# Kernel optimization log

Hardware: AMD Instinct MI355X
Metric: run time of the kernel (lower is better)

The kernel has to match this reference:

```python
import jax, jax.numpy as jnp
import numpy as np

B, IMG, TXT = 1, 2048, 256
D_MODEL = 2048
HEADS, HEAD_DIM = 16, 128
INNER = HEADS * HEAD_DIM
EPS = 1e-5
SCALE = HEAD_DIM ** -0.5


def _rmsnorm(x, w):
    # normalize over last dim (head_dim)
    return (x * jax.lax.rsqrt(jnp.mean(x * x, axis=-1, keepdims=True) + EPS)) * w


def _rope(x, cos, sin):
    # x: (B, S, H, D); cos/sin: (S, D) with pairwise-repeated freqs (interleaved convention)
    c = cos[None, :, None, :]
    s = sin[None, :, None, :]
    x1 = x[..., 0::2]
    x2 = x[..., 1::2]
    rot = jnp.stack([-x2, x1], axis=-1).reshape(x.shape)
    return x * c + rot * s


def setup_inputs() -> dict:
    key = jax.random.key(0)
    ks = jax.random.split(key, 12)
    sc_in = D_MODEL ** -0.5
    sc_inner = INNER ** -0.5
    inp = {
        'hidden_states': jax.random.normal(ks[0], (B, IMG, D_MODEL), jnp.float32),
        'encoder_hidden_states': jax.random.normal(ks[1], (B, TXT, D_MODEL), jnp.float32),
    }
    # RoPE tables over the joint (text + image) sequence, interleaved pair layout
    pos = jnp.arange(TXT + IMG, dtype=jnp.float32)
    inv = 1.0 / (10000.0 ** (jnp.arange(0, HEAD_DIM, 2, dtype=jnp.float32) / HEAD_DIM))
    freqs = pos[:, None] * inv[None, :]
    freqs = jnp.repeat(freqs, 2, axis=-1)  # (S, HEAD_DIM)
    inp['freqs_cos'] = jnp.cos(freqs)
    inp['freqs_sin'] = jnp.sin(freqs)
    # parameters (stored (in, out))
    inp['Wqkv'] = jax.random.normal(ks[2], (D_MODEL, 3 * INNER), jnp.float32) * sc_in
    inp['Wqkv_add'] = jax.random.normal(ks[3], (D_MODEL, 3 * INNER), jnp.float32) * sc_in
    inp['b_qkv_add'] = jax.random.normal(ks[4], (3 * INNER,), jnp.float32) * 0.01
    inp['norm_q_w'] = jnp.ones((HEAD_DIM,), jnp.float32)
    inp['norm_k_w'] = jnp.ones((HEAD_DIM,), jnp.float32)
    inp['norm_aq_w'] = jnp.ones((HEAD_DIM,), jnp.float32)
    inp['norm_ak_w'] = jnp.ones((HEAD_DIM,), jnp.float32)
    inp['Wout'] = jax.random.normal(ks[5], (INNER, D_MODEL), jnp.float32) * sc_inner
    inp['b_out'] = jax.random.normal(ks[6], (D_MODEL,), jnp.float32) * 0.01
    inp['Wadd_out'] = jax.random.normal(ks[7], (INNER, D_MODEL), jnp.float32) * sc_inner
    inp['b_add_out'] = jax.random.normal(ks[8], (D_MODEL,), jnp.float32) * 0.01
    return inp


def reference(hidden_states, encoder_hidden_states, freqs_cos, freqs_sin,
              Wqkv, Wqkv_add, b_qkv_add, norm_q_w, norm_k_w, norm_aq_w, norm_ak_w,
              Wout, b_out, Wadd_out, b_add_out):
    b, s_img, _ = hidden_states.shape
    s_txt = encoder_hidden_states.shape[1]

    # fused QKV projection (image stream), chunk q/k/v, unflatten heads
    qkv = hidden_states @ Wqkv  # (B, IMG, 3*INNER)
    q, k, v = jnp.split(qkv, 3, axis=-1)
    q = _rmsnorm(q.reshape(b, s_img, HEADS, HEAD_DIM), norm_q_w)
    k = _rmsnorm(k.reshape(b, s_img, HEADS, HEAD_DIM), norm_k_w)
    v = v.reshape(b, s_img, HEADS, HEAD_DIM)

    # fused QKV projection (text stream, with bias)
    eqkv = encoder_hidden_states @ Wqkv_add + b_qkv_add
    eq, ek, ev = jnp.split(eqkv, 3, axis=-1)
    eq = _rmsnorm(eq.reshape(b, s_txt, HEADS, HEAD_DIM), norm_aq_w)
    ek = _rmsnorm(ek.reshape(b, s_txt, HEADS, HEAD_DIM), norm_ak_w)
    ev = ev.reshape(b, s_txt, HEADS, HEAD_DIM)

    # joint [text; image] concatenation, then RoPE on joint Q/K
    jq = jnp.concatenate([eq, q], axis=1)
    jk = jnp.concatenate([ek, k], axis=1)
    jv = jnp.concatenate([ev, v], axis=1)
    jq = _rope(jq, freqs_cos, freqs_sin)
    jk = _rope(jk, freqs_cos, freqs_sin)

    # non-causal scaled dot-product attention, layout (B, S, H, D)
    scores = jnp.einsum('bqhd,bkhd->bhqk', jq, jk) * SCALE
    probs = jax.nn.softmax(scores, axis=-1)
    out = jnp.einsum('bhqk,bkhd->bqhd', probs, jv)  # (B, S_joint, H, D)
    out = out.reshape(b, s_txt + s_img, INNER)

    enc_out = out[:, :s_txt]
    img_out = out[:, s_txt:]
    img_out = img_out @ Wout + b_out
    enc_out = enc_out @ Wadd_out + b_add_out
    return (img_out, enc_out)
```

## Files before the change

kernel.cpp:

```cpp
#include <hip/hip_runtime.h>
#include <stdint.h>

#define HEADS 16
#define HD 128
#define S_TXT 256
#define S_IMG 2048
#define S_ALL 2304
#define DMODEL 2048
#define N_QKV 6144
#define INNER 2048
#define ATT_EPS 1e-5f
#define ATT_SCALE 0.08838834764831845f
#define LOG2E 1.4426950408889634f
#define MBOUND 16.5f
#define QT_N 18
#define TPS 36

typedef __attribute__((ext_vector_type(8))) __bf16 bf16x8;
typedef __attribute__((ext_vector_type(4))) float f32x4;
typedef __attribute__((ext_vector_type(4))) uint32_t u32x4;

__device__ __forceinline__ uint16_t f2bf(float f) {
  union { float f; uint32_t u; } v; v.f = f;
  uint32_t r = (v.u + 0x7FFF + ((v.u >> 16) & 1)) >> 16;
  return (uint16_t)r;
}
__device__ __forceinline__ float bf2f(uint16_t h) {
  union { float f; uint32_t u; } v; v.u = ((uint32_t)h) << 16;
  return v.f;
}
__device__ __forceinline__ float fexp2(float x) {
#if __has_builtin(__builtin_amdgcn_exp2f)
  return __builtin_amdgcn_exp2f(x);
#else
  return __expf(x * 0.69314718055994531f);
#endif
}

__device__ __forceinline__ void async_cp16(const void* g, void* l) {
  __builtin_amdgcn_global_load_lds(
      (const __attribute__((address_space(1))) void*)g,
      (__attribute__((address_space(3))) void*)l, 16, 0, 0);
}

__global__ __launch_bounds__(256) void k_cvt2(
    const float* __restrict__ s0, uint16_t* __restrict__ d0, int n40,
    const float* __restrict__ s1, uint16_t* __restrict__ d1, int n41) {
  const float* src; uint16_t* dst; int n4, bid, nb;
  if (blockIdx.x < 1024) { src = s0; dst = d0; n4 = n40; bid = blockIdx.x; nb = 1024; }
  else { src = s1; dst = d1; n4 = n41; bid = blockIdx.x - 1024; nb = 128; }
  int i = bid * 256 + threadIdx.x;
  int stride = nb * 256;
  for (; i < n4; i += stride) {
    float4 v = ((const float4*)src)[i];
    uint16_t o[4];
    o[0] = f2bf(v.x); o[1] = f2bf(v.y); o[2] = f2bf(v.z); o[3] = f2bf(v.w);
    ((uint2*)dst)[i] = *(const uint2*)o;
  }
}

__global__ __launch_bounds__(256) void k_cvt_t4(
    const float* __restrict__ s0, uint16_t* __restrict__ d0,
    const float* __restrict__ s1, uint16_t* __restrict__ d1,
    const float* __restrict__ s2, uint16_t* __restrict__ d2,
    const float* __restrict__ s3, uint16_t* __restrict__ d3) {
  __shared__ float t[64][65];
  int b = blockIdx.x;
  const float* src; uint16_t* dst; int R, C, tb;
  if (b < 3072)      { src = s0; dst = d0; R = DMODEL; C = N_QKV;  tb = b; }
  else if (b < 6144) { src = s1; dst = d1; R = DMODEL; C = N_QKV;  tb = b - 3072; }
  else if (b < 7168) { src = s2; dst = d2; R = INNER;  C = DMODEL; tb = b - 6144; }
  else               { src = s3; dst = d3; R = INNER;  C = DMODEL; tb = b - 7168; }
  int ntr = R >> 6;
  int tr = tb % ntr, tc = tb / ntr;
  int tid = threadIdx.x;
  int rr = tid >> 4, c4 = (tid & 15) * 4;
#pragma unroll
  for (int j = 0; j < 4; ++j) {
    int r = rr + j * 16;
    float4 v = *(const float4*)&src[(size_t)(tr * 64 + r) * C + tc * 64 + c4];
    *(float4*)&t[r][c4] = v;
  }
  __syncthreads();
  int cc = tid >> 4, r4 = (tid & 15) * 4;
#pragma unroll
  for (int j = 0; j < 4; ++j) {
    int c = cc + j * 16;
    uint16_t ov[4];
    ov[0] = f2bf(t[r4 + 0][c]); ov[1] = f2bf(t[r4 + 1][c]);
    ov[2] = f2bf(t[r4 + 2][c]); ov[3] = f2bf(t[r4 + 3][c]);
    *(uint2*)&dst[(size_t)(tc * 64 + c) * R + tr * 64 + r4] = *(const uint2*)ov;
  }
}

__global__ __launch_bounds__(512, 1) void k_gemm2(
    const uint16_t* __restrict__ A0, const uint16_t* __restrict__ B0,
    const float* __restrict__ bias0, uint16_t* __restrict__ C0,
    const uint16_t* __restrict__ A1, const uint16_t* __restrict__ B1,
    const float* __restrict__ bias1, uint16_t* __restrict__ C1,
    int seg0_tiles, int N, int K) {
  __shared__ __align__(16) char lds[2 * 65536];
  int bn = blockIdx.x, bm = blockIdx.y;
  const uint16_t* A; const uint16_t* B; const float* bias; uint16_t* C; int mrow;
  if (bm < seg0_tiles) { A = A0; B = B0; bias = bias0; C = C0; mrow = bm * 256; }
  else { A = A1; B = B1; bias = bias1; C = C1; mrow = (bm - seg0_tiles) * 256; }
  int tid = threadIdx.x, lane = tid & 63, w = tid >> 6;
  int g = lane >> 4, li = lane & 15;
  int wm = w >> 2, wn = w & 3;
  const int NKI = K / 64;

  int rowin = lane >> 3;
  int csrc = (lane & 7) ^ rowin;

  auto stage = [&](int t, char* buf) {
    int kt = t * 64;
#pragma unroll
    for (int j = 0; j < 4; ++j) {
      int r = w * 4 + j;
      int tr = r * 8 + rowin;
      async_cp16(A + (size_t)(mrow + tr) * K + kt + 8 * csrc, buf + r * 1024);
    }
#pragma unroll
    for (int j = 0; j < 4; ++j) {
      int r = w * 4 + j;
      int tr = r * 8 + rowin;
      async_cp16(B + (size_t)(bn * 256 + tr) * K + kt + 8 * csrc, buf + 32768 + r * 1024);
    }
  };

  f32x4 acc[8][4] = {};

  stage(0, lds);
  asm volatile("s_waitcnt vmcnt(0)" ::: "memory");
  __builtin_amdgcn_s_barrier();
  asm volatile("" ::: "memory");

  for (int t = 0; t < NKI; ++t) {
    const char* cur = lds + (t & 1) * 65536;
    if (t + 1 < NKI) stage(t + 1, lds + ((t + 1) & 1) * 65536);

#pragma unroll
    for (int kk = 0; kk < 2; ++kk) {
      bf16x8 af[8], bfv[4];
#pragma unroll
      for (int mi = 0; mi < 8; ++mi) {
        int row = wm * 128 + mi * 16 + li;
        int ch = (kk * 4 + g) ^ (row & 7);
        af[mi] = __builtin_bit_cast(bf16x8, *(const u32x4*)(cur + row * 128 + ch * 16));
      }
#pragma unroll
      for (int ni = 0; ni < 4; ++ni) {
        int row = wn * 64 + ni * 16 + li;
        int ch = (kk * 4 + g) ^ (row & 7);
        bfv[ni] = __builtin_bit_cast(bf16x8, *(const u32x4*)(cur + 32768 + row * 128 + ch * 16));
      }
      __builtin_amdgcn_s_setprio(1);
#pragma unroll
      for (int mi = 0; mi < 8; ++mi)
#pragma unroll
        for (int ni = 0; ni < 4; ++ni)
          acc[mi][ni] = __builtin_amdgcn_mfma_f32_16x16x32_bf16(af[mi], bfv[ni], acc[mi][ni], 0, 0, 0);
      __builtin_amdgcn_s_setprio(0);
    }

    if (t + 1 < NKI) {
      asm volatile("s_waitcnt vmcnt(0)" ::: "memory");
      __builtin_amdgcn_s_barrier();
      asm volatile("" ::: "memory");
    }
  }

#pragma unroll
  for (int mi = 0; mi < 8; ++mi) {
#pragma unroll
    for (int ni = 0; ni < 4; ++ni) {
      int col = bn * 256 + wn * 64 + ni * 16 + li;
      float bv = bias ? bias[col] : 0.0f;
#pragma unroll
      for (int i = 0; i < 4; ++i) {
        int r = mrow + wm * 128 + mi * 16 + 4 * g + i;
        C[(size_t)r * N + col] = f2bf(acc[mi][ni][i] + bv);
      }
    }
  }
}

__global__ __launch_bounds__(256, 4) void k_gemmO(
    const uint16_t* __restrict__ A0, const uint16_t* __restrict__ B0,
    const float* __restrict__ bias0, float* __restrict__ C0,
    const uint16_t* __restrict__ A1, const uint16_t* __restrict__ B1,
    const float* __restrict__ bias1, float* __restrict__ C1,
    int seg0_tiles, int N, int K) {
  __shared__ __align__(16) char lds[4 * 8192];
  int bn = blockIdx.x, bm = blockIdx.y;
  const uint16_t* A; const uint16_t* B; const float* bias; float* C; int mrow;
  if (bm < seg0_tiles) { A = A0; B = B0; bias = bias0; C = C0; mrow = bm * 128; }
  else { A = A1; B = B1; bias = bias1; C = C1; mrow = (bm - seg0_tiles) * 128; }
  int tid = threadIdx.x, lane = tid & 63, w = tid >> 6;
  int g = lane >> 4, li = lane & 15;
  int wm = w >> 1, wn = w & 1;
  const int NKT = K / 32;

  int rowin = lane >> 2;
  int csrc = (lane & 3) ^ (rowin & 3);

  auto stage = [&](int t, int buf) {
    int kt = t * 32;
#pragma unroll
    for (int j = 0; j < 2; ++j) {
      int r = w * 2 + j;
      int tr = r * 16 + rowin;
      async_cp16(A + (size_t)(mrow + tr) * K + kt + 8 * csrc, lds + buf * 8192 + r * 1024);
    }
#pragma unroll
    for (int j = 0; j < 2; ++j) {
      int r = w * 2 + j;
      int tr = r * 16 + rowin;
      async_cp16(B + (size_t)(bn * 128 + tr) * K + kt + 8 * csrc, lds + 16384 + buf * 8192 + r * 1024);
    }
  };

  f32x4 acc[4][4] = {};
  stage(0, 0);
  asm volatile("s_waitcnt vmcnt(0)" ::: "memory");
  __builtin_amdgcn_s_barrier();
  asm volatile("" ::: "memory");

  for (int t = 0; t < NKT; ++t) {
    int cur = t & 1;
    bool pre = (t + 1 < NKT);
    if (pre) stage(t + 1, cur ^ 1);
    const char* Ac = lds + cur * 8192;
    const char* Bc = lds + 16384 + cur * 8192;

    bf16x8 af[4], bfv[4];
#pragma unroll
    for (int mi = 0; mi < 4; ++mi) {
      int row = wm * 64 + mi * 16 + li;
      af[mi] = __builtin_bit_cast(bf16x8, *(const u32x4*)(Ac + row * 64 + (g ^ (row & 3)) * 16));
    }
#pragma unroll
    for (int ni = 0; ni < 4; ++ni) {
      int row = wn * 64 + ni * 16 + li;
      bfv[ni] = __builtin_bit_cast(bf16x8, *(const u32x4*)(Bc + row * 64 + (g ^ (row & 3)) * 16));
    }
    __builtin_amdgcn_s_setprio(1);
#pragma unroll
    for (int mi = 0; mi < 4; ++mi)
#pragma unroll
      for (int ni = 0; ni < 4; ++ni)
        acc[mi][ni] = __builtin_amdgcn_mfma_f32_16x16x32_bf16(af[mi], bfv[ni], acc[mi][ni], 0, 0, 0);
    __builtin_amdgcn_s_setprio(0);

    if (pre) asm volatile("s_waitcnt vmcnt(0)" ::: "memory");
    __builtin_amdgcn_s_barrier();
    asm volatile("" ::: "memory");
  }

#pragma unroll
  for (int mi = 0; mi < 4; ++mi) {
#pragma unroll
    for (int ni = 0; ni < 4; ++ni) {
      int col = bn * 128 + wn * 64 + ni * 16 + li;
      float bv = bias[col];
#pragma unroll
      for (int i = 0; i < 4; ++i) {
        int r = mrow + wm * 64 + mi * 16 + 4 * g + i;
        C[(size_t)r * N + col] = acc[mi][ni][i] + bv;
      }
    }
  }
}

__global__ __launch_bounds__(256) void k_postvt(
    const uint16_t* __restrict__ qkv_img, const uint16_t* __restrict__ qkv_txt,
    const float* __restrict__ fcos, const float* __restrict__ fsin,
    const float* __restrict__ wq, const float* __restrict__ wk,
    const float* __restrict__ waq, const float* __restrict__ wak,
    uint16_t* __restrict__ Qo, uint16_t* __restrict__ Ko, uint16_t* __restrict__ VTo) {
  __shared__ uint16_t Vl[64][136];
  if (blockIdx.x < S_ALL) {
    int s = blockIdx.x;
    const uint16_t* row = (s < S_TXT) ? qkv_txt + (size_t)s * N_QKV
                                      : qkv_img + (size_t)(s - S_TXT) * N_QKV;
    const float* wqp = (s < S_TXT) ? waq : wq;
    const float* wkp = (s < S_TXT) ? wak : wk;
    int lane = threadIdx.x & 63, w = threadIdx.x >> 6;
    int h = w * 4 + (lane >> 4);
    int d0 = (lane & 15) * 8;
    float cs[8], sn[8];
#pragma unroll
    for (int j = 0; j < 8; ++j) {
      cs[j] = fcos[s * HD + d0 + j];
      sn[j] = fsin[s * HD + d0 + j];
    }
#pragma unroll
    for (int part = 0; part < 2; ++part) {
      const uint16_t* src = row + part * INNER + h * HD + d0;
      u32x4 raw = *(const u32x4*)src;
      const uint16_t* rp = (const uint16_t*)&raw;
      float x[8], ss = 0.f;
#pragma unroll
      for (int j = 0; j < 8; ++j) { x[j] = bf2f(rp[j]); ss += x[j] * x[j]; }
      ss += __shfl_xor(ss, 1); ss += __shfl_xor(ss, 2);
      ss += __shfl_xor(ss, 4); ss += __shfl_xor(ss, 8);
      float rn = rsqrtf(ss * (1.0f / HD) + ATT_EPS);
      const float* wp = part ? wkp : wqp;
#pragma unroll
      for (int j = 0; j < 8; ++j) x[j] = x[j] * rn * wp[d0 + j];
      float y[8];
#pragma unroll
      for (int j = 0; j < 8; j += 2) {
        y[j]     = x[j] * cs[j] - x[j + 1] * sn[j];
        y[j + 1] = x[j + 1] * cs[j + 1] + x[j] * sn[j + 1];
      }
      float sc = part ? 1.0f : (ATT_SCALE * LOG2E);
      uint16_t ov[8];
#pragma unroll
      for (int j = 0; j < 8; ++j) ov[j] = f2bf(y[j] * sc);
      uint16_t* dst = (part ? Ko : Qo) + ((size_t)h * S_ALL + s) * HD + d0;
      *(u32x4*)dst = *(const u32x4*)ov;
    }
  } else {
    int b = blockIdx.x - S_ALL;
    int st = b % 36, h = b / 36;
    int s0 = st * 64;
    const uint16_t* base = (s0 < S_TXT) ? qkv_txt + (size_t)s0 * N_QKV
                                        : qkv_img + (size_t)(s0 - S_TXT) * N_QKV;
    base += 2 * INNER + h * HD;
    int tid = threadIdx.x;
#pragma unroll
    for (int it = 0; it < 4; ++it) {
      int idx = it * 256 + tid;
      int r = idx >> 4, c = idx & 15;
      *(u32x4*)&Vl[r][c * 8] = *(const u32x4*)(base + (size_t)r * N_QKV + c * 8);
    }
    __syncthreads();
#pragma unroll
    for (int it = 0; it < 4; ++it) {
      int idx = it * 256 + tid;
      int d = idx >> 3, sc = (idx & 7) * 8;
      uint16_t tmp[8];
#pragma unroll
      for (int j = 0; j < 8; ++j) tmp[j] = Vl[sc + j][d];
      *(u32x4*)&VTo[((size_t)h * HD + d) * S_ALL + s0 + sc] = *(const u32x4*)tmp;
    }
  }
}

__global__ __launch_bounds__(256, 3) void k_attn(
    const uint16_t* __restrict__ Qg, const uint16_t* __restrict__ Kg,
    const uint16_t* __restrict__ VTg,
    uint16_t* __restrict__ part0, uint16_t* __restrict__ part1,
    float* __restrict__ lsumP) {
  __shared__ __align__(16) char Kt[2][8192];
  __shared__ __align__(16) char Vt[2][8192];
  __shared__ __align__(16) uint16_t Pl[4][32 * 40];

  int b0 = blockIdx.x;
  int bid = (b0 & 7) * 72 + (b0 >> 3);
  int h = bid / 36, r6 = bid % 36, sp = r6 / 18, qt = r6 % 18;
  int tid = threadIdx.x, lane = tid & 63, w = tid >> 6;
  int g = lane >> 4, li = lane & 15;

  const uint16_t* Kh = Kg + (size_t)h * S_ALL * HD;
  const uint16_t* Vh = VTg + (size_t)h * HD * S_ALL;
  uint16_t* po = (sp ? part1 : part0) + ((size_t)(h * QT_N + qt) * 128 + w * 32) * 128;

  int qbase = qt * 128 + w * 32;
  bf16x8 qf[2][4];
#pragma unroll
  for (int q2 = 0; q2 < 2; ++q2) {
    const uint16_t* qp = Qg + ((size_t)h * S_ALL + qbase + q2 * 16 + li) * HD;
#pragma unroll
    for (int kc = 0; kc < 4; ++kc)
      qf[q2][kc] = __builtin_bit_cast(bf16x8, *(const u32x4*)(qp + kc * 32 + g * 8));
  }
  f32x4 o[2][8] = {};
  float lsum[2] = {0.f, 0.f};

  auto stage = [&](int tk, int buf) {
#pragma unroll
    for (int j = 0; j < 2; ++j) {
      int cj = w * 128 + j * 64 + lane;
      int row = cj >> 4, c = (cj & 15) ^ (row & 15);
      async_cp16(Kh + (size_t)(tk * 32 + row) * HD + 8 * c, Kt[buf] + (w * 128 + j * 64) * 16);
    }
#pragma unroll
    for (int j = 0; j < 2; ++j) {
      int cj = w * 128 + j * 64 + lane;
      int row = cj >> 2, c = (cj & 3) ^ ((row >> 1) & 3);
      async_cp16(Vh + (size_t)row * S_ALL + tk * 32 + 8 * c, Vt[buf] + (w * 128 + j * 64) * 16);
    }
  };

  int t0 = sp * TPS;
  stage(t0, 0);
  asm volatile("s_waitcnt vmcnt(0)" ::: "memory");
  __builtin_amdgcn_s_barrier();
  asm volatile("" ::: "memory");

  for (int t = 0; t < TPS; ++t) {
    int cur = t & 1;
    if (t + 1 < TPS) stage(t0 + t + 1, cur ^ 1);
    const char* KtC = Kt[cur];
    const char* VtC = Vt[cur];

    f32x4 sc[2][2];
#pragma unroll
    for (int q2 = 0; q2 < 2; ++q2)
#pragma unroll
      for (int kb = 0; kb < 2; ++kb)
        sc[q2][kb] = (f32x4){-MBOUND, -MBOUND, -MBOUND, -MBOUND};
    __builtin_amdgcn_s_setprio(1);
#pragma unroll
    for (int kb = 0; kb < 2; ++kb)
#pragma unroll
      for (int kc = 0; kc < 4; ++kc) {
        int ch = (kc * 4 + g) ^ li;
        bf16x8 kf = __builtin_bit_cast(bf16x8,
            *(const u32x4*)(KtC + (kb * 16 + li) * 256 + ch * 16));
        sc[0][kb] = __builtin_amdgcn_mfma_f32_16x16x32_bf16(kf, qf[0][kc], sc[0][kb], 0, 0, 0);
        sc[1][kb] = __builtin_amdgcn_mfma_f32_16x16x32_bf16(kf, qf[1][kc], sc[1][kb], 0, 0, 0);
      }
    __builtin_amdgcn_s_setprio(0);

    uint16_t* Pw = &Pl[w][0];
#pragma unroll
    for (int q2 = 0; q2 < 2; ++q2)
#pragma unroll
      for (int kb = 0; kb < 2; ++kb) {
        float p0 = fexp2(sc[q2][kb][0]);
        float p1 = fexp2(sc[q2][kb][1]);
        float p2 = fexp2(sc[q2][kb][2]);
        float p3 = fexp2(sc[q2][kb][3]);
        lsum[q2] += (p0 + p1) + (p2 + p3);
        uint2 pk;
        pk.x = (uint32_t)f2bf(p0) | ((uint32_t)f2bf(p1) << 16);
        pk.y = (uint32_t)f2bf(p2) | ((uint32_t)f2bf(p3) << 16);
        *(uint2*)((char*)Pw + (q2 * 16 + li) * 80 + kb * 32 + g * 8) = pk;
      }

    bf16x8 pf[2];
#pragma unroll
    for (int q2 = 0; q2 < 2; ++q2)
      pf[q2] = __builtin_bit_cast(bf16x8,
          *(const u32x4*)((const char*)Pw + (q2 * 16 + li) * 80 + g * 16));
    __builtin_amdgcn_s_setprio(1);
#pragma unroll
    for (int db = 0; db < 8; ++db) {
      int vrow = db * 16 + li;
      int ch = g ^ ((vrow >> 1) & 3);
      bf16x8 vf = __builtin_bit_cast(bf16x8, *(const u32x4*)(VtC + vrow * 64 + ch * 16));
      o[0][db] = __builtin_amdgcn_mfma_f32_16x16x32_bf16(pf[0], vf, o[0][db], 0, 0, 0);
      o[1][db] = __builtin_amdgcn_mfma_f32_16x16x32_bf16(pf[1], vf, o[1][db], 0, 0, 0);
    }
    __builtin_amdgcn_s_setprio(0);

    asm volatile("s_waitcnt vmcnt(0)" ::: "memory");
    __builtin_amdgcn_s_barrier();
    asm volatile("" ::: "memory");
  }

#pragma unroll
  for (int q2 = 0; q2 < 2; ++q2) {
    float v = lsum[q2];
    v += __shfl_xor(v, 16);
    v += __shfl_xor(v, 32);
    lsum[q2] = v;
  }
  if (lane < 16) {
#pragma unroll
    for (int q2 = 0; q2 < 2; ++q2)
      lsumP[((size_t)sp * HEADS + h) * S_ALL + qbase + q2 * 16 + lane] = lsum[q2];
  }
#pragma unroll
  for (int q2 = 0; q2 < 2; ++q2)
#pragma unroll
    for (int db = 0; db < 8; ++db)
#pragma unroll
      for (int i = 0; i < 4; ++i)
        po[(q2 * 16 + 4 * g + i) * 128 + db * 16 + li] = f2bf(o[q2][db][i]);
}

__global__ __launch_bounds__(256) void k_comb(
    const uint16_t* __restrict__ p0, const uint16_t* __restrict__ p1,
    const float* __restrict__ lsumP, uint16_t* __restrict__ attn) {
  int q = blockIdx.x, qt = q >> 7, ql = q & 127;
#pragma unroll
  for (int rep = 0; rep < 2; ++rep) {
    int d4 = threadIdx.x + rep * 256;
    int d = d4 * 4, h = d >> 7, dl = d & 127;
    size_t off = (((size_t)h * QT_N + qt) * 128 + ql) * 128 + dl;
    uint2 a = *(const uint2*)&p0[off];
    uint2 b = *(const uint2*)&p1[off];
    const uint16_t* ap = (const uint16_t*)&a;
    const uint16_t* bp = (const uint16_t*)&b;
    float l0 = lsumP[(size_t)h * S_ALL + q];
    float l1 = lsumP[((size_t)HEADS + h) * S_ALL + q];
    float inv = 1.0f / (l0 + l1);
    uint16_t ov[4];
#pragma unroll
    for (int j = 0; j < 4; ++j)
      ov[j] = f2bf((bf2f(ap[j]) + bf2f(bp[j])) * inv);
    *(uint2*)&attn[(size_t)q * INNER + d] = *(const uint2*)ov;
  }
}

extern "C" void kernel_launch(void* const* d_in, const int* in_sizes, int n_in,
                              void* d_out, int out_size, void* d_ws, size_t ws_size,
                              hipStream_t stream) {
  const float* hidden = (const float*)d_in[0];
  const float* enc    = (const float*)d_in[1];
  const float* fcos   = (const float*)d_in[2];
  const float* fsin   = (const float*)d_in[3];
  const float* Wqkv   = (const float*)d_in[4];
  const float* Wqkva  = (const float*)d_in[5];
  const float* bqkva  = (const float*)d_in[6];
  const float* nqw    = (const float*)d_in[7];
  const float* nkw    = (const float*)d_in[8];
  const float* naqw   = (const float*)d_in[9];
  const float* nakw   = (const float*)d_in[10];
  const float* Wout   = (const float*)d_in[11];
  const float* bout   = (const float*)d_in[12];
  const float* Wadd   = (const float*)d_in[13];
  const float* badd   = (const float*)d_in[14];
  float* out_img = (float*)d_out;
  float* out_enc = (float*)d_out + (size_t)S_IMG * DMODEL;

  char* ws = (char*)d_ws;
  size_t off = 0;
  auto alloc = [&](size_t bytes) {
    char* p = ws + off;
    off += (bytes + 255) & ~(size_t)255;
    return p;
  };
  uint16_t* hs_bf   = (uint16_t*)alloc((size_t)S_IMG * DMODEL * 2);
  uint16_t* enc_bf  = (uint16_t*)alloc((size_t)S_TXT * DMODEL * 2);
  char*     wqkv_base = alloc((size_t)N_QKV * DMODEL * 2 * 2);
  uint16_t* WqkvT   = (uint16_t*)wqkv_base;
  uint16_t* WqkvaT  = (uint16_t*)(wqkv_base + (size_t)N_QKV * DMODEL * 2);
  uint16_t* WoutT   = (uint16_t*)alloc((size_t)DMODEL * INNER * 2);
  uint16_t* WaddT   = (uint16_t*)alloc((size_t)DMODEL * INNER * 2);
  uint16_t* qkv_img = (uint16_t*)alloc((size_t)S_IMG * N_QKV * 2);
  uint16_t* qkv_txt = (uint16_t*)alloc((size_t)S_TXT * N_QKV * 2);
  uint16_t* Qb   = (uint16_t*)wqkv_base;
  uint16_t* Kb   = Qb + (size_t)HEADS * S_ALL * HD;
  uint16_t* VTb  = Kb + (size_t)HEADS * S_ALL * HD;
  uint16_t* attn = VTb + (size_t)HEADS * S_ALL * HD;
  uint16_t* part0 = (uint16_t*)d_out;
  uint16_t* part1 = (uint16_t*)qkv_img;
  float* lsumP = (float*)enc_bf;

  k_cvt2<<<1152, 256, 0, stream>>>(hidden, hs_bf, S_IMG * DMODEL / 4,
                                   enc, enc_bf, S_TXT * DMODEL / 4);
  k_cvt_t4<<<8192, 256, 0, stream>>>(Wqkv, WqkvT, Wqkva, WqkvaT, Wout, WoutT, Wadd, WaddT);

  dim3 gq(N_QKV / 256, (S_TXT + S_IMG) / 256);
  k_gemm2<<<gq, 512, 0, stream>>>(enc_bf, WqkvaT, bqkva, qkv_txt,
                                  hs_bf, WqkvT, nullptr, qkv_img,
                                  1, N_QKV, DMODEL);

  k_postvt<<<S_ALL + 36 * HEADS, 256, 0, stream>>>(qkv_img, qkv_txt, fcos, fsin,
                                                   nqw, nkw, naqw, nakw, Qb, Kb, VTb);

  k_attn<<<HEADS * QT_N * 2, 256, 0, stream>>>(Qb, Kb, VTb, part0, part1, lsumP);
  k_comb<<<S_ALL, 256, 0, stream>>>(part0, part1, lsumP, attn);

  dim3 go(DMODEL / 128, S_ALL / 128);
  k_gemmO<<<go, 256, 0, stream>>>(attn, WaddT, badd, out_enc,
                                  attn + (size_t)S_TXT * INNER, WoutT, bout, out_img,
                                  2, DMODEL, DMODEL);
}
```

Before: 217.5 us.

## Split attention KV range four ways and use packed bf16 conversion instruction

Attention now splits each head's key sequence into four partitions instead of two (TPS halved), launching twice as many blocks and writing four partial outputs that the combine kernel sums with four partial row sums. This aims to raise occupancy and balance across the GPU's compute units for the attention stage, at the cost of more partial-output traffic and extra workspace aliasing into the output buffer. Separately, manual round-to-nearest bf16 packing is replaced with the hardware v_cvt_pk_bf16_f32 instruction in the conversion kernels and the P-matrix packing.

```diff
diff --git a/kernel.cpp b/kernel.cpp
--- a/kernel.cpp
+++ b/kernel.cpp
@@ -14,7 +14,7 @@
 #define LOG2E 1.4426950408889634f
 #define MBOUND 16.5f
 #define QT_N 18
-#define TPS 36
+#define TPS 18
 
 typedef __attribute__((ext_vector_type(8))) __bf16 bf16x8;
 typedef __attribute__((ext_vector_type(4))) float f32x4;
@@ -28,6 +28,11 @@
 __device__ __forceinline__ float bf2f(uint16_t h) {
   union { float f; uint32_t u; } v; v.u = ((uint32_t)h) << 16;
   return v.f;
+}
+__device__ __forceinline__ uint32_t cvt_pk_bf16(float lo, float hi) {
+  uint32_t r;
+  asm("v_cvt_pk_bf16_f32 %0, %1, %2" : "=v"(r) : "v"(lo), "v"(hi));
+  return r;
 }
 __device__ __forceinline__ float fexp2(float x) {
 #if __has_builtin(__builtin_amdgcn_exp2f)
@@ -53,9 +58,10 @@
   int stride = nb * 256;
   for (; i < n4; i += stride) {
     float4 v = ((const float4*)src)[i];
-    uint16_t o[4];
-    o[0] = f2bf(v.x); o[1] = f2bf(v.y); o[2] = f2bf(v.z); o[3] = f2bf(v.w);
-    ((uint2*)dst)[i] = *(const uint2*)o;
+    uint2 o;
+    o.x = cvt_pk_bf16(v.x, v.y);
+    o.y = cvt_pk_bf16(v.z, v.w);
+    ((uint2*)dst)[i] = o;
   }
 }
 
@@ -86,10 +92,10 @@
 #pragma unroll
   for (int j = 0; j < 4; ++j) {
     int c = cc + j * 16;
-    uint16_t ov[4];
-    ov[0] = f2bf(t[r4 + 0][c]); ov[1] = f2bf(t[r4 + 1][c]);
-    ov[2] = f2bf(t[r4 + 2][c]); ov[3] = f2bf(t[r4 + 3][c]);
-    *(uint2*)&dst[(size_t)(tc * 64 + c) * R + tr * 64 + r4] = *(const uint2*)ov;
+    uint2 o;
+    o.x = cvt_pk_bf16(t[r4 + 0][c], t[r4 + 1][c]);
+    o.y = cvt_pk_bf16(t[r4 + 2][c], t[r4 + 3][c]);
+    *(uint2*)&dst[(size_t)(tc * 64 + c) * R + tr * 64 + r4] = o;
   }
 }
 
@@ -352,20 +358,22 @@
     const uint16_t* __restrict__ Qg, const uint16_t* __restrict__ Kg,
     const uint16_t* __restrict__ VTg,
     uint16_t* __restrict__ part0, uint16_t* __restrict__ part1,
+    uint16_t* __restrict__ part2, uint16_t* __restrict__ part3,
     float* __restrict__ lsumP) {
   __shared__ __align__(16) char Kt[2][8192];
   __shared__ __align__(16) char Vt[2][8192];
   __shared__ __align__(16) uint16_t Pl[4][32 * 40];
 
   int b0 = blockIdx.x;
-  int bid = (b0 & 7) * 72 + (b0 >> 3);
-  int h = bid / 36, r6 = bid % 36, sp = r6 / 18, qt = r6 % 18;
+  int bid = (b0 & 7) * 144 + (b0 >> 3);
+  int h = bid / 72, r6 = bid % 72, sp = r6 / 18, qt = r6 % 18;
   int tid = threadIdx.x, lane = tid & 63, w = tid >> 6;
   int g = lane >> 4, li = lane & 15;
 
   const uint16_t* Kh = Kg + (size_t)h * S_ALL * HD;
   const uint16_t* Vh = VTg + (size_t)h * HD * S_ALL;
-  uint16_t* po = (sp ? part1 : part0) + ((size_t)(h * QT_N + qt) * 128 + w * 32) * 128;
+  uint16_t* po = (sp & 2) ? ((sp & 1) ? part3 : part2) : ((sp & 1) ? part1 : part0);
+  po += ((size_t)(h * QT_N + qt) * 128 + w * 32) * 128;
 
   int qbase = qt * 128 + w * 32;
   bf16x8 qf[2][4];
@@ -436,8 +444,8 @@
         float p3 = fexp2(sc[q2][kb][3]);
         lsum[q2] += (p0 + p1) + (p2 + p3);
         uint2 pk;
-        pk.x = (uint32_t)f2bf(p0) | ((uint32_t)f2bf(p1) << 16);
-        pk.y = (uint32_t)f2bf(p2) | ((uint32_t)f2bf(p3) << 16);
+        pk.x = cvt_pk_bf16(p0, p1);
+        pk.y = cvt_pk_bf16(p2, p3);
         *(uint2*)((char*)Pw + (q2 * 16 + li) * 80 + kb * 32 + g * 8) = pk;
       }
 
@@ -485,6 +493,7 @@
 
 __global__ __launch_bounds__(256) void k_comb(
     const uint16_t* __restrict__ p0, const uint16_t* __restrict__ p1,
+    const uint16_t* __restrict__ p2, const uint16_t* __restrict__ p3,
     const float* __restrict__ lsumP, uint16_t* __restrict__ attn) {
   int q = blockIdx.x, qt = q >> 7, ql = q & 127;
 #pragma unroll
@@ -494,15 +503,21 @@
     size_t off = (((size_t)h * QT_N + qt) * 128 + ql) * 128 + dl;
     uint2 a = *(const uint2*)&p0[off];
     uint2 b = *(const uint2*)&p1[off];
+    uint2 c = *(const uint2*)&p2[off];
+    uint2 e = *(const uint2*)&p3[off];
     const uint16_t* ap = (const uint16_t*)&a;
     const uint16_t* bp = (const uint16_t*)&b;
-    float l0 = lsumP[(size_t)h * S_ALL + q];
-    float l1 = lsumP[((size_t)HEADS + h) * S_ALL + q];
-    float inv = 1.0f / (l0 + l1);
+    const uint16_t* cp = (const uint16_t*)&c;
+    const uint16_t* ep = (const uint16_t*)&e;
+    float l = 0.f;
+#pragma unroll
+    for (int s = 0; s < 4; ++s)
+      l += lsumP[((size_t)s * HEADS + h) * S_ALL + q];
+    float inv = 1.0f / l;
     uint16_t ov[4];
 #pragma unroll
     for (int j = 0; j < 4; ++j)
-      ov[j] = f2bf((bf2f(ap[j]) + bf2f(bp[j])) * inv);
+      ov[j] = f2bf((bf2f(ap[j]) + bf2f(bp[j]) + bf2f(cp[j]) + bf2f(ep[j])) * inv);
     *(uint2*)&attn[(size_t)q * INNER + d] = *(const uint2*)ov;
   }
 }
@@ -549,7 +564,9 @@
   uint16_t* VTb  = Kb + (size_t)HEADS * S_ALL * HD;
   uint16_t* attn = VTb + (size_t)HEADS * S_ALL * HD;
   uint16_t* part0 = (uint16_t*)d_out;
-  uint16_t* part1 = (uint16_t*)qkv_img;
+  uint16_t* part1 = part0 + (size_t)S_ALL * INNER;
+  uint16_t* part2 = (uint16_t*)qkv_img;
+  uint16_t* part3 = part2 + (size_t)S_ALL * INNER;
   float* lsumP = (float*)enc_bf;
 
   k_cvt2<<<1152, 256, 0, stream>>>(hidden, hs_bf, S_IMG * DMODEL / 4,
@@ -564,8 +581,8 @@
   k_postvt<<<S_ALL + 36 * HEADS, 256, 0, stream>>>(qkv_img, qkv_txt, fcos, fsin,
                                                    nqw, nkw, naqw, nakw, Qb, Kb, VTb);
 
-  k_attn<<<HEADS * QT_N * 2, 256, 0, stream>>>(Qb, Kb, VTb, part0, part1, lsumP);
-  k_comb<<<S_ALL, 256, 0, stream>>>(part0, part1, lsumP, attn);
+  k_attn<<<HEADS * QT_N * 4, 256, 0, stream>>>(Qb, Kb, VTb, part0, part1, part2, part3, lsumP);
+  k_comb<<<S_ALL, 256, 0, stream>>>(part0, part1, part2, part3, lsumP, attn);
 
   dim3 go(DMODEL / 128, S_ALL / 128);
   k_gemmO<<<go, 256, 0, stream>>>(attn, WaddT, badd, out_enc,
```

Result: faster. 211.5 us (-2.8%).
